# Performance work log

Hardware: AMD Instinct MI355X
Metric: run time of the kernel (lower is better)

Reference implementation:

```python
import jax, jax.numpy as jnp
import numpy as np

N_NODES = 50000
N_EDGES = 800000
IN_CH, HID_CH, OUT_CH = 128, 128, 64


def _gcn_conv(x, W, b, src, dst, n):
    """PyG GCNConv: self-loops + symmetric norm + linear + scatter-add + bias."""
    loop = jnp.arange(n, dtype=src.dtype)
    src_sl = jnp.concatenate([src, loop])  # [E+N]
    dst_sl = jnp.concatenate([dst, loop])
    # degree computed on edges incl. self-loops (edge weight 1)
    deg = jax.ops.segment_sum(jnp.ones_like(dst_sl, dtype=x.dtype), dst_sl,
                              num_segments=n)
    dinv = jnp.where(deg > 0, jax.lax.rsqrt(deg), 0.0)
    norm = dinv[src_sl] * dinv[dst_sl]  # [E+N]
    xw = x @ W  # [N, F_out]
    msg = xw[src_sl] * norm[:, None]  # gather + scale, [E+N, F_out]
    out = jax.ops.segment_sum(msg, dst_sl, num_segments=n)
    return out + b


def setup_inputs() -> dict:
    key = jax.random.key(0)
    ks = jax.random.split(key, 5)
    x = jax.random.normal(ks[0], (N_NODES, IN_CH), dtype=jnp.float32)
    edge_index = jax.random.randint(ks[1], (2, N_EDGES), 0, N_NODES, dtype=jnp.int64)
    s1 = 1.0 / np.sqrt(IN_CH)
    s2 = 1.0 / np.sqrt(HID_CH)
    W1 = jax.random.normal(ks[2], (IN_CH, HID_CH), dtype=jnp.float32) * s1
    W2 = jax.random.normal(ks[3], (HID_CH, HID_CH), dtype=jnp.float32) * s2
    W3 = jax.random.normal(ks[4], (HID_CH, OUT_CH), dtype=jnp.float32) * s2
    return {
        "x": x, "edge_index": edge_index,
        "W1": W1, "b1": jnp.zeros((HID_CH,), jnp.float32),
        "W2": W2, "b2": jnp.zeros((HID_CH,), jnp.float32),
        "W3": W3, "b3": jnp.zeros((OUT_CH,), jnp.float32),
    }


def reference(x, edge_index, W1, b1, W2, b2, W3, b3):
    n = x.shape[0]
    src, dst = edge_index[0], edge_index[1]
    # dropout(p=0.6) is identity in eval mode
    h = jax.nn.relu(_gcn_conv(x, W1, b1, src, dst, n))
    h = jax.nn.relu(_gcn_conv(h, W2, b2, src, dst, n))
    out = _gcn_conv(h, W3, b3, src, dst, n)
    return out
```

## Files before the change

### kernel.cpp

```cpp
#include <hip/hip_runtime.h>
#include <cstdint>

#define CAP 32768
#define CHUNK 2048

typedef __attribute__((ext_vector_type(8))) short bf8_t;
typedef __attribute__((ext_vector_type(4))) float f4_t;

__device__ __forceinline__ uint32_t f_to_bf(float f) {
    union { float f; uint32_t u; } v; v.f = f;
    uint32_t u = v.u;
    return (u + 0x7fffu + ((u >> 16) & 1u)) >> 16;
}
__device__ __forceinline__ float bf_to_f(uint32_t h) {
    union { uint32_t u; float f; } v; v.u = h << 16; return v.f;
}
__device__ __forceinline__ float2 bf2_to_f2(uint32_t u) {
    union { uint32_t u; float f; } a, b;
    a.u = u << 16; b.u = u & 0xffff0000u;
    float2 r; r.x = a.f; r.y = b.f; return r;
}
__device__ __forceinline__ void fma8(float* acc, uint4 u, float d) {
    float2 p0 = bf2_to_f2(u.x), p1 = bf2_to_f2(u.y);
    float2 p2 = bf2_to_f2(u.z), p3 = bf2_to_f2(u.w);
    acc[0] += p0.x * d; acc[1] += p0.y * d;
    acc[2] += p1.x * d; acc[3] += p1.y * d;
    acc[4] += p2.x * d; acc[5] += p2.y * d;
    acc[6] += p3.x * d; acc[7] += p3.y * d;
}

__device__ __forceinline__ int detect64(const int* __restrict__ e32) {
    return (e32[1] | e32[3] | e32[5] | e32[7]) == 0;
}
__device__ __forceinline__ int edge_at(const void* edges, int is64, int idx) {
    if (is64) return (int)((const long long*)edges)[idx];
    return ((const int*)edges)[idx];
}

__device__ __forceinline__ void wsplit_body(
    int idx, const float* __restrict__ W1, const float* __restrict__ W2,
    const float* __restrict__ W3,
    uint16_t* w1h, uint16_t* w1l, uint16_t* w2h, uint16_t* w2l,
    uint16_t* w3h, uint16_t* w3l) {
    const float* W; uint16_t* oh; uint16_t* ol; int FOUT; int e;
    if (idx < 16384)      { W = W1; oh = w1h; ol = w1l; FOUT = 128; e = idx; }
    else if (idx < 32768) { W = W2; oh = w2h; ol = w2l; FOUT = 128; e = idx - 16384; }
    else                  { W = W3; oh = w3h; ol = w3l; FOUT = 64;  e = idx - 32768; }
    int j = e & 7;
    int lane = (e >> 3) & 63;
    int rem = e >> 9;
    int NT = FOUT >> 4;
    int nt = rem % NT, kc = rem / NT;
    int k = kc * 32 + ((lane >> 4) << 3) + j;
    int c = nt * 16 + (lane & 15);
    float v = W[(size_t)k * FOUT + c];
    uint32_t h = f_to_bf(v);
    uint32_t l = f_to_bf(v - bf_to_f(h));
    oh[e] = (uint16_t)h;
    ol[e] = (uint16_t)l;
}

__global__ __launch_bounds__(256) void scatter_wprep_kernel(
    const void* __restrict__ ei, int* __restrict__ bucket_cur,
    int2* __restrict__ buckets, int E, int sbcnt,
    const float* __restrict__ W1, const float* __restrict__ W2,
    const float* __restrict__ W3,
    uint16_t* w1h, uint16_t* w1l, uint16_t* w2h, uint16_t* w2l,
    uint16_t* w3h, uint16_t* w3l) {
    int tid = threadIdx.x;
    if ((int)blockIdx.x >= sbcnt) {
        int idx = (blockIdx.x - sbcnt) * 256 + tid;
        wsplit_body(idx, W1, W2, W3, w1h, w1l, w2h, w2l, w3h, w3l);
        return;
    }
    __shared__ int cnt[64];
    int base = blockIdx.x * CHUNK;
    int is64 = detect64((const int*)ei);
    if (tid < 64) cnt[tid] = 0;
    __syncthreads();
    int dloc[8], sloc[8];
#pragma unroll
    for (int it = 0; it < 8; it++) {
        int i = base + it * 256 + tid;
        int d = (i < E) ? edge_at(ei, is64, E + i) : -1;
        int s = (i < E) ? edge_at(ei, is64, i) : 0;
        dloc[it] = d;
        sloc[it] = s;
        if (d >= 0) atomicAdd(&cnt[d >> 10], 1);
    }
    __syncthreads();
    if (tid < 64) {
        int v = cnt[tid];
        cnt[tid] = atomicAdd(&bucket_cur[tid], v);
    }
    __syncthreads();
#pragma unroll
    for (int it = 0; it < 8; it++) {
        if (dloc[it] >= 0) {
            int b = dloc[it] >> 10;
            int p = atomicAdd(&cnt[b], 1);
            buckets[(size_t)b * CAP + p] = make_int2(sloc[it], dloc[it]);
        }
    }
}

__device__ __forceinline__ void gemm1_body(
    const float* __restrict__ A, const uint16_t* __restrict__ Wfhi,
    const uint16_t* __restrict__ Wflo, uint16_t* __restrict__ Yout,
    int n, int wid, int tile0, int tstride, int lane,
    uint16_t* __restrict__ hs, uint16_t* __restrict__ ls) {
    constexpr int NT = 8, NTW = 2, LDW = 136;
    int ntiles = (n + 15) >> 4;
    bf8_t wh[NTW][4], wl[NTW][4];
#pragma unroll
    for (int t = 0; t < NTW; t++) {
        int nt = wid * NTW + t;
#pragma unroll
        for (int kc = 0; kc < 4; kc++) {
            size_t b = ((size_t)(kc * NT + nt) * 64 + lane) * 8;
            wh[t][kc] = *(const bf8_t*)&Wfhi[b];
            wl[t][kc] = *(const bf8_t*)&Wflo[b];
        }
    }
    int row_in = lane & 15;
    int koff = (lane >> 4) << 3;
    int colb = lane & 15;
    int rq = (lane >> 4) << 2;
    int kcw = wid;
    float4 pv = {0, 0, 0, 0}, qv = {0, 0, 0, 0};
    if (tile0 < ntiles) {
        int arow = (tile0 << 4) + row_in; if (arow >= n) arow = n - 1;
        const float* ap = A + (size_t)arow * 128 + kcw * 32 + koff;
        pv = *(const float4*)ap;
        qv = *(const float4*)(ap + 4);
    }
    for (int tile = tile0; tile < ntiles; tile += tstride) {
        int R = tile << 4;
        {
            float vv[8] = {pv.x, pv.y, pv.z, pv.w, qv.x, qv.y, qv.z, qv.w};
            bf8_t H, L;
#pragma unroll
            for (int j = 0; j < 8; j++) {
                uint32_t h = f_to_bf(vv[j]);
                H[j] = (short)h;
                L[j] = (short)f_to_bf(vv[j] - bf_to_f(h));
            }
            *(bf8_t*)&hs[row_in * LDW + kcw * 32 + koff] = H;
            *(bf8_t*)&ls[row_in * LDW + kcw * 32 + koff] = L;
        }
        __syncthreads();
        int tnext = tile + tstride;
        if (tnext < ntiles) {
            int arow2 = (tnext << 4) + row_in; if (arow2 >= n) arow2 = n - 1;
            const float* ap2 = A + (size_t)arow2 * 128 + kcw * 32 + koff;
            pv = *(const float4*)ap2;
            qv = *(const float4*)(ap2 + 4);
        }
        bf8_t ah[4], al[4];
#pragma unroll
        for (int kc = 0; kc < 4; kc++) {
            ah[kc] = *(const bf8_t*)&hs[(lane & 15) * LDW + koff + kc * 32];
            al[kc] = *(const bf8_t*)&ls[(lane & 15) * LDW + koff + kc * 32];
        }
        f4_t acc[NTW];
#pragma unroll
        for (int t = 0; t < NTW; t++) acc[t] = (f4_t){0.f, 0.f, 0.f, 0.f};
#pragma unroll
        for (int kc = 0; kc < 4; kc++) {
#pragma unroll
            for (int t = 0; t < NTW; t++) {
                acc[t] = __builtin_amdgcn_mfma_f32_16x16x32_bf16(ah[kc], wh[t][kc], acc[t], 0, 0, 0);
                acc[t] = __builtin_amdgcn_mfma_f32_16x16x32_bf16(ah[kc], wl[t][kc], acc[t], 0, 0, 0);
                acc[t] = __builtin_amdgcn_mfma_f32_16x16x32_bf16(al[kc], wh[t][kc], acc[t], 0, 0, 0);
            }
        }
#pragma unroll
        for (int t = 0; t < NTW; t++) {
            int c = (wid * NTW + t) * 16 + colb;
#pragma unroll
            for (int r = 0; r < 4; r++) {
                int row = R + rq + r;
                if (row < n)
                    Yout[(size_t)row * 128 + c] = (uint16_t)f_to_bf(acc[t][r]);
            }
        }
        __syncthreads();
    }
}

__global__ __launch_bounds__(256) void csrfill_gemm1_kernel(
    const int2* __restrict__ buckets, const int* __restrict__ bucket_cur,
    int* __restrict__ row_ptr, int* __restrict__ col,
    float* __restrict__ dinv, int nbuck,
    const float* __restrict__ x, const uint16_t* __restrict__ w1h,
    const uint16_t* __restrict__ w1l, uint16_t* __restrict__ y1, int n) {
    __shared__ __align__(16) char smem[12288];
    __shared__ int s_bo;
    int tid = threadIdx.x;
    if ((int)blockIdx.x >= nbuck) {
        uint16_t* hs = (uint16_t*)smem;
        uint16_t* ls = (uint16_t*)(smem + 4352);
        int lane = tid & 63, wid = tid >> 6;
        gemm1_body(x, w1h, w1l, y1, n, wid, blockIdx.x - nbuck,
                   gridDim.x - nbuck, lane, hs, ls);
        return;
    }
    int* cnt = (int*)smem;
    int* sb  = (int*)(smem + 4096);
    int* cur = (int*)(smem + 8192);
    int b = blockIdx.x;
    int base = b << 10;
    int lim = min(1024, n - base);
    if (tid < 64) {
        int v = (tid < nbuck) ? bucket_cur[tid] : 0;
        int incl = v;
#pragma unroll
        for (int off = 1; off < 64; off <<= 1) {
            int t = __shfl_up(incl, off);
            if (tid >= off) incl += t;
        }
        int tot = __shfl(incl, nbuck - 1);
        int bo = (b > 0) ? __shfl(incl, b - 1) : 0;
        if (tid == 0) {
            s_bo = bo;
            if (b == nbuck - 1) row_ptr[n] = tot;
        }
    }
    int ecnt = bucket_cur[b];
    const int2* ebase = buckets + (size_t)b * CAP;
    for (int i = tid; i < 1024; i += 256) cnt[i] = 0;
    __syncthreads();
    {
        int i = tid;
        for (; i + 768 < ecnt; i += 1024) {
            int y0 = ebase[i].y;
            int y1_ = ebase[i + 256].y;
            int y2_ = ebase[i + 512].y;
            int y3_ = ebase[i + 768].y;
            atomicAdd(&cnt[y0 - base], 1);
            atomicAdd(&cnt[y1_ - base], 1);
            atomicAdd(&cnt[y2_ - base], 1);
            atomicAdd(&cnt[y3_ - base], 1);
        }
        for (; i < ecnt; i += 256)
            atomicAdd(&cnt[ebase[i].y - base], 1);
    }
    __syncthreads();
    for (int i = tid; i < lim; i += 256)
        dinv[base + i] = rsqrtf((float)(cnt[i] + 1));
    __syncthreads();
    int* a = cnt; int* s = sb;
    for (int st = 1; st < 1024; st <<= 1) {
        for (int i = tid; i < 1024; i += 256)
            s[i] = a[i] + ((i >= st) ? a[i - st] : 0);
        __syncthreads();
        int* t = a; a = s; s = t;
    }
    int bo = s_bo;
    for (int i = tid; i < lim; i += 256) {
        int v = ((i > 0) ? a[i - 1] : 0) + bo;
        row_ptr[base + i] = v;
        cur[i] = v;
    }
    __syncthreads();
    {
        int i = tid;
        for (; i + 768 < ecnt; i += 1024) {
            int2 e0 = ebase[i];
            int2 e1 = ebase[i + 256];
            int2 e2 = ebase[i + 512];
            int2 e3 = ebase[i + 768];
            int p0 = atomicAdd(&cur[e0.y - base], 1); col[p0] = e0.x;
            int p1 = atomicAdd(&cur[e1.y - base], 1); col[p1] = e1.x;
            int p2 = atomicAdd(&cur[e2.y - base], 1); col[p2] = e2.x;
            int p3 = atomicAdd(&cur[e3.y - base], 1); col[p3] = e3.x;
        }
        for (; i < ecnt; i += 256) {
            int2 e = ebase[i];
            int p = atomicAdd(&cur[e.y - base], 1);
            col[p] = e.x;
        }
    }
}

template <int FOUT, bool SRC_SCALE>
__global__ __launch_bounds__(256) void agg_gemm_kernel(
    const uint16_t* __restrict__ Yin, const int* __restrict__ row_ptr,
    const int* __restrict__ col, const float* __restrict__ dinv,
    const float* __restrict__ bias,
    const uint16_t* __restrict__ Wfhi, const uint16_t* __restrict__ Wflo,
    uint16_t* __restrict__ Yout, int n) {
    __shared__ uint4 hs4[16 * 17];
    __shared__ uint4 ls4[16 * 17];
    int tid = threadIdx.x, wid = tid >> 6, lane = tid & 63;
    int base = blockIdx.x * 16;
    int g = lane & 15, j = lane >> 4;
    const uint4* Y4 = (const uint4*)Yin;

    float4 bb0 = *(const float4*)&bias[g * 8];
    float4 bb1 = *(const float4*)&bias[g * 8 + 4];
    float bb[8] = {bb0.x, bb0.y, bb0.z, bb0.w, bb1.x, bb1.y, bb1.z, bb1.w};

    for (int q = 0; q < 4; q++) {
        int r = wid * 4 + q, node = base + r;
        uint4 ph = (uint4){0, 0, 0, 0}, pl = (uint4){0, 0, 0, 0};
        if (node < n) {
            float di = dinv[node];
            float aA[8] = {}, aB[8] = {};
            {
                float sd = (j == 0) ? (SRC_SCALE ? di : 1.f) : 0.f;
                uint4 su = Y4[(size_t)node * 16 + g];
                fma8(aA, su, sd);
            }
            int start = row_ptr[node], end = row_ptr[node + 1];
            for (int b = start; b < end; b += 64) {
                int cnt = min(64, end - b);
                int sv = (b + lane < end) ? col[b + lane] : 0;
                for (int k = 0; k < cnt; k += 8) {
                    int iA = k + j, iB = k + 4 + j;
                    int sA = __shfl(sv, iA & 63);
                    int sB = __shfl(sv, iB & 63);
                    float dA = (iA < cnt) ? (SRC_SCALE ? dinv[sA] : 1.f) : 0.f;
                    float dB = (iB < cnt) ? (SRC_SCALE ? dinv[sB] : 1.f) : 0.f;
                    uint4 uA = Y4[(size_t)sA * 16 + g];
                    uint4 uB = Y4[(size_t)sB * 16 + g];
                    fma8(aA, uA, dA);
                    fma8(aB, uB, dB);
                }
            }
            float o[8];
#pragma unroll
            for (int t = 0; t < 8; t++) o[t] = aA[t] + aB[t];
#pragma unroll
            for (int t = 0; t < 8; t++) o[t] += __shfl_xor(o[t], 16);
#pragma unroll
            for (int t = 0; t < 8; t++) o[t] += __shfl_xor(o[t], 32);
            uint32_t hh[8];
#pragma unroll
            for (int t = 0; t < 8; t++) {
                o[t] = fmaxf(o[t] * di + bb[t], 0.f);
                hh[t] = f_to_bf(o[t]);
            }
            ph = (uint4){hh[0] | (hh[1] << 16), hh[2] | (hh[3] << 16),
                         hh[4] | (hh[5] << 16), hh[6] | (hh[7] << 16)};
            uint32_t ll[8];
#pragma unroll
            for (int t = 0; t < 8; t++) ll[t] = f_to_bf(o[t] - bf_to_f(hh[t]));
            pl = (uint4){ll[0] | (ll[1] << 16), ll[2] | (ll[3] << 16),
                         ll[4] | (ll[5] << 16), ll[6] | (ll[7] << 16)};
        }
        if (j == 0) {
            hs4[r * 17 + g] = ph;
            ls4[r * 17 + g] = pl;
        }
    }
    __syncthreads();

    const uint16_t* hs = (const uint16_t*)hs4;
    const uint16_t* ls = (const uint16_t*)ls4;
    constexpr int NT = FOUT / 16;
    constexpr int NTW = NT / 4;
    constexpr int LDW = 136;
    int cp = wid;
    bf8_t wh[NTW][4], wl[NTW][4];
#pragma unroll
    for (int t = 0; t < NTW; t++) {
        int nt = cp * NTW + t;
#pragma unroll
        for (int kc = 0; kc < 4; kc++) {
            size_t b = ((size_t)(kc * NT + nt) * 64 + lane) * 8;
            wh[t][kc] = *(const bf8_t*)&Wfhi[b];
            wl[t][kc] = *(const bf8_t*)&Wflo[b];
        }
    }
    int koff = (lane >> 4) << 3;
    int colb = lane & 15;
    int rq = (lane >> 4) << 2;
    bf8_t ah[4], al[4];
#pragma unroll
    for (int kc = 0; kc < 4; kc++) {
        ah[kc] = *(const bf8_t*)(hs + (lane & 15) * LDW + koff + kc * 32);
        al[kc] = *(const bf8_t*)(ls + (lane & 15) * LDW + koff + kc * 32);
    }
    f4_t acc[NTW];
#pragma unroll
    for (int t = 0; t < NTW; t++) acc[t] = (f4_t){0.f, 0.f, 0.f, 0.f};
#pragma unroll
    for (int kc = 0; kc < 4; kc++) {
#pragma unroll
        for (int t = 0; t < NTW; t++) {
            acc[t] = __builtin_amdgcn_mfma_f32_16x16x32_bf16(ah[kc], wh[t][kc], acc[t], 0, 0, 0);
            acc[t] = __builtin_amdgcn_mfma_f32_16x16x32_bf16(ah[kc], wl[t][kc], acc[t], 0, 0, 0);
            acc[t] = __builtin_amdgcn_mfma_f32_16x16x32_bf16(al[kc], wh[t][kc], acc[t], 0, 0, 0);
        }
    }
#pragma unroll
    for (int t = 0; t < NTW; t++) {
        int c = (cp * NTW + t) * 16 + colb;
#pragma unroll
        for (int r = 0; r < 4; r++) {
            int row = base + rq + r;
            if (row < n) {
                float v = acc[t][r] * dinv[row];
                Yout[(size_t)row * FOUT + c] = (uint16_t)f_to_bf(v);
            }
        }
    }
}

__global__ __launch_bounds__(256) void agg_final_kernel(
    const uint16_t* __restrict__ Y, const int* __restrict__ row_ptr,
    const int* __restrict__ col, const float* __restrict__ dinv,
    const float* __restrict__ bias, float* __restrict__ out, int n) {
    int w = blockIdx.x * 4 + (threadIdx.x >> 6);
    int lane = threadIdx.x & 63;
    if (w >= n) return;
    int g = lane & 7, j = lane >> 3;
    const uint4* Y4 = (const uint4*)Y;
    float4 bb0 = *(const float4*)&bias[g * 8];
    float4 bb1 = *(const float4*)&bias[g * 8 + 4];
    float bb[8] = {bb0.x, bb0.y, bb0.z, bb0.w, bb1.x, bb1.y, bb1.z, bb1.w};

    float aA[8] = {}, aB[8] = {};
    {
        uint4 su = Y4[(size_t)w * 8 + g];
        fma8(aA, su, (j == 0) ? 1.f : 0.f);
    }
    int start = row_ptr[w], end = row_ptr[w + 1];
    for (int b = start; b < end; b += 64) {
        int cnt = min(64, end - b);
        int sv = (b + lane < end) ? col[b + lane] : 0;
        for (int k = 0; k < cnt; k += 16) {
            int iA = k + j, iB = k + 8 + j;
            int sA = __shfl(sv, iA & 63);
            int sB = __shfl(sv, iB & 63);
            float dA = (iA < cnt) ? 1.f : 0.f;
            float dB = (iB < cnt) ? 1.f : 0.f;
            uint4 uA = Y4[(size_t)sA * 8 + g];
            uint4 uB = Y4[(size_t)sB * 8 + g];
            fma8(aA, uA, dA);
            fma8(aB, uB, dB);
        }
    }
    float o[8];
#pragma unroll
    for (int t = 0; t < 8; t++) o[t] = aA[t] + aB[t];
#pragma unroll
    for (int t = 0; t < 8; t++) o[t] += __shfl_xor(o[t], 8);
#pragma unroll
    for (int t = 0; t < 8; t++) o[t] += __shfl_xor(o[t], 16);
#pragma unroll
    for (int t = 0; t < 8; t++) o[t] += __shfl_xor(o[t], 32);
    float di = dinv[w];
#pragma unroll
    for (int t = 0; t < 8; t++) o[t] = o[t] * di + bb[t];
    if (j == 0) {
        float4 o0 = {o[0], o[1], o[2], o[3]};
        float4 o1 = {o[4], o[5], o[6], o[7]};
        *(float4*)&out[(size_t)w * 64 + g * 8] = o0;
        *(float4*)&out[(size_t)w * 64 + g * 8 + 4] = o1;
    }
}

extern "C" void kernel_launch(void* const* d_in, const int* in_sizes, int n_in,
                              void* d_out, int out_size, void* d_ws, size_t ws_size,
                              hipStream_t stream) {
    const float* x  = (const float*)d_in[0];
    const void*  ei = d_in[1];
    const float* W1 = (const float*)d_in[2];
    const float* b1 = (const float*)d_in[3];
    const float* W2 = (const float*)d_in[4];
    const float* b2 = (const float*)d_in[5];
    const float* W3 = (const float*)d_in[6];
    const float* b3 = (const float*)d_in[7];
    int n = in_sizes[0] / 128;
    int E = in_sizes[1] / 2;
    int nbuck = (n + 1023) >> 10;

    char* p = (char*)d_ws;
    auto carve = [&](size_t bytes) {
        char* r = p;
        p += (bytes + 255) & ~(size_t)255;
        return r;
    };
    float*    dinv       = (float*)carve((size_t)n * 4);
    int*      row_ptr    = (int*)carve((size_t)(n + 1) * 4);
    int*      bucket_cur = (int*)carve(64 * 4);
    int*      col        = (int*)carve((size_t)E * 4);
    int2*     buckets    = (int2*)carve((size_t)64 * CAP * 8);
    uint16_t* y1         = (uint16_t*)carve((size_t)n * 128 * 2);
    uint16_t* y2         = (uint16_t*)carve((size_t)n * 128 * 2);
    uint16_t* y3         = (uint16_t*)carve((size_t)n * 64 * 2);
    uint16_t* w1h        = (uint16_t*)carve(128 * 128 * 2);
    uint16_t* w1l        = (uint16_t*)carve(128 * 128 * 2);
    uint16_t* w2h        = (uint16_t*)carve(128 * 128 * 2);
    uint16_t* w2l        = (uint16_t*)carve(128 * 128 * 2);
    uint16_t* w3h        = (uint16_t*)carve(128 * 64 * 2);
    uint16_t* w3l        = (uint16_t*)carve(128 * 64 * 2);

    int sbcnt = (E + CHUNK - 1) / CHUNK;
    int fb = (n + 15) / 16;

    hipMemsetAsync(bucket_cur, 0, 64 * 4, stream);
    scatter_wprep_kernel<<<sbcnt + 160, 256, 0, stream>>>(
        ei, bucket_cur, buckets, E, sbcnt,
        W1, W2, W3, w1h, w1l, w2h, w2l, w3h, w3l);
    csrfill_gemm1_kernel<<<nbuck + 782, 256, 0, stream>>>(
        buckets, bucket_cur, row_ptr, col, dinv, nbuck,
        x, w1h, w1l, y1, n);
    agg_gemm_kernel<128, true><<<fb, 256, 0, stream>>>(
        y1, row_ptr, col, dinv, b1, w2h, w2l, y2, n);
    agg_gemm_kernel<64, false><<<fb, 256, 0, stream>>>(
        y2, row_ptr, col, dinv, b2, w3h, w3l, y3, n);
    agg_final_kernel<<<(n + 3) / 4, 256, 0, stream>>>(
        y3, row_ptr, col, dinv, b3, (float*)d_out, n);
}
```

Measured before the change: 230.4 us.

## Reformulate neighbor aggregation as sparse-weight MFMA over staged edge rows

The per-node gather-and-FMA aggregation is replaced by a block-wide scheme. Chunks of 64 CSR edges for the block's 16 nodes are staged into shared memory, a 16x64 selection matrix of bf16 hi/lo edge weights is built, and the aggregation runs as MFMA products, with self-loops handled as a diagonal pass. This aims to move the aggregation onto matrix cores and improve gather coalescing. In exchange it adds several __syncthreads per chunk, shared-memory zeroing, a binary search per edge, and strided transposed LDS reads for the B fragments.

```diff
diff --git a/kernel.cpp b/kernel.cpp
--- a/kernel.cpp
+++ b/kernel.cpp
@@ -290,118 +290,195 @@
     const float* __restrict__ bias,
     const uint16_t* __restrict__ Wfhi, const uint16_t* __restrict__ Wflo,
     uint16_t* __restrict__ Yout, int n) {
-    __shared__ uint4 hs4[16 * 17];
-    __shared__ uint4 ls4[16 * 17];
+    constexpr int RLD = 136;
+    constexpr int SLD = 72;
+    __shared__ uint16_t rows[64 * RLD];
+    __shared__ uint16_t Shi[16 * SLD];
+    __shared__ uint16_t Slo[16 * SLD];
+    __shared__ uint16_t hs[16 * 136];
+    __shared__ uint16_t ls[16 * 136];
+    __shared__ int   s_rp[17];
+    __shared__ float s_di[16];
+    __shared__ float s_bias[128];
+
     int tid = threadIdx.x, wid = tid >> 6, lane = tid & 63;
     int base = blockIdx.x * 16;
-    int g = lane & 15, j = lane >> 4;
+    int grp = lane & 15;
     const uint4* Y4 = (const uint4*)Yin;
 
-    float4 bb0 = *(const float4*)&bias[g * 8];
-    float4 bb1 = *(const float4*)&bias[g * 8 + 4];
-    float bb[8] = {bb0.x, bb0.y, bb0.z, bb0.w, bb1.x, bb1.y, bb1.z, bb1.w};
-
-    for (int q = 0; q < 4; q++) {
-        int r = wid * 4 + q, node = base + r;
-        uint4 ph = (uint4){0, 0, 0, 0}, pl = (uint4){0, 0, 0, 0};
-        if (node < n) {
-            float di = dinv[node];
-            float aA[8] = {}, aB[8] = {};
-            {
-                float sd = (j == 0) ? (SRC_SCALE ? di : 1.f) : 0.f;
-                uint4 su = Y4[(size_t)node * 16 + g];
-                fma8(aA, su, sd);
-            }
-            int start = row_ptr[node], end = row_ptr[node + 1];
-            for (int b = start; b < end; b += 64) {
-                int cnt = min(64, end - b);
-                int sv = (b + lane < end) ? col[b + lane] : 0;
-                for (int k = 0; k < cnt; k += 8) {
-                    int iA = k + j, iB = k + 4 + j;
-                    int sA = __shfl(sv, iA & 63);
-                    int sB = __shfl(sv, iB & 63);
-                    float dA = (iA < cnt) ? (SRC_SCALE ? dinv[sA] : 1.f) : 0.f;
-                    float dB = (iB < cnt) ? (SRC_SCALE ? dinv[sB] : 1.f) : 0.f;
-                    uint4 uA = Y4[(size_t)sA * 16 + g];
-                    uint4 uB = Y4[(size_t)sB * 16 + g];
-                    fma8(aA, uA, dA);
-                    fma8(aB, uB, dB);
+    if (tid < 17) {
+        int idx = base + tid; if (idx > n) idx = n;
+        s_rp[tid] = row_ptr[idx];
+    }
+    if (tid >= 32 && tid < 48) {
+        int m = tid - 32;
+        s_di[m] = (base + m < n) ? dinv[base + m] : 0.f;
+    }
+    if (tid >= 64 && tid < 192) s_bias[tid - 64] = bias[tid - 64];
+    {
+        uint4* r4 = (uint4*)rows;
+        for (int i = tid; i < 64 * RLD / 8; i += 256) r4[i] = (uint4){0, 0, 0, 0};
+    }
+    __syncthreads();
+
+    int e0 = s_rp[0], e1 = s_rp[16];
+    f4_t acc[2] = {(f4_t){0.f, 0.f, 0.f, 0.f}, (f4_t){0.f, 0.f, 0.f, 0.f}};
+
+    for (int cb = e0; cb < e1; cb += 64) {
+        int cnt = min(64, e1 - cb);
+        int sv = (cb + lane < e1) ? col[cb + lane] : 0;
+        for (int i = tid; i < (16 * SLD) / 8; i += 256) {
+            ((uint4*)Shi)[i] = (uint4){0, 0, 0, 0};
+            ((uint4*)Slo)[i] = (uint4){0, 0, 0, 0};
+        }
+        __syncthreads();
+        if (wid == 0 && lane < cnt) {
+            int e = cb + lane;
+            int lo = 0, hi = 16;
+            while (hi - lo > 1) {
+                int mid = (lo + hi) >> 1;
+                if (s_rp[mid] <= e) lo = mid; else hi = mid;
+            }
+            float w = SRC_SCALE ? dinv[sv] : 1.f;
+            uint32_t h = f_to_bf(w);
+            Shi[lo * SLD + lane] = (uint16_t)h;
+            if (SRC_SCALE)
+                Slo[lo * SLD + lane] = (uint16_t)f_to_bf(w - bf_to_f(h));
+        }
+#pragma unroll
+        for (int i = 0; i < 4; i++) {
+            int slot = wid * 16 + i * 4 + (lane >> 4);
+            int src = __shfl(sv, slot);
+            if (slot < cnt) {
+                uint4 u = Y4[(size_t)src * 16 + grp];
+                *(uint4*)&rows[slot * RLD + grp * 8] = u;
+            }
+        }
+        __syncthreads();
+#pragma unroll
+        for (int t = 0; t < 2; t++) {
+            int nt = wid * 2 + t;
+#pragma unroll
+            for (int kc = 0; kc < 2; kc++) {
+                int kb = kc * 32 + ((lane >> 4) << 3);
+                bf8_t bfrag;
+#pragma unroll
+                for (int j = 0; j < 8; j++)
+                    bfrag[j] = (short)rows[(kb + j) * RLD + nt * 16 + grp];
+                bf8_t ah = *(const bf8_t*)&Shi[grp * SLD + kb];
+                acc[t] = __builtin_amdgcn_mfma_f32_16x16x32_bf16(ah, bfrag, acc[t], 0, 0, 0);
+                if (SRC_SCALE) {
+                    bf8_t al = *(const bf8_t*)&Slo[grp * SLD + kb];
+                    acc[t] = __builtin_amdgcn_mfma_f32_16x16x32_bf16(al, bfrag, acc[t], 0, 0, 0);
                 }
             }
-            float o[8];
-#pragma unroll
-            for (int t = 0; t < 8; t++) o[t] = aA[t] + aB[t];
-#pragma unroll
-            for (int t = 0; t < 8; t++) o[t] += __shfl_xor(o[t], 16);
-#pragma unroll
-            for (int t = 0; t < 8; t++) o[t] += __shfl_xor(o[t], 32);
-            uint32_t hh[8];
-#pragma unroll
-            for (int t = 0; t < 8; t++) {
-                o[t] = fmaxf(o[t] * di + bb[t], 0.f);
-                hh[t] = f_to_bf(o[t]);
-            }
-            ph = (uint4){hh[0] | (hh[1] << 16), hh[2] | (hh[3] << 16),
-                         hh[4] | (hh[5] << 16), hh[6] | (hh[7] << 16)};
-            uint32_t ll[8];
-#pragma unroll
-            for (int t = 0; t < 8; t++) ll[t] = f_to_bf(o[t] - bf_to_f(hh[t]));
-            pl = (uint4){ll[0] | (ll[1] << 16), ll[2] | (ll[3] << 16),
-                         ll[4] | (ll[5] << 16), ll[6] | (ll[7] << 16)};
-        }
-        if (j == 0) {
-            hs4[r * 17 + g] = ph;
-            ls4[r * 17 + g] = pl;
-        }
-    }
-    __syncthreads();
-
-    const uint16_t* hs = (const uint16_t*)hs4;
-    const uint16_t* ls = (const uint16_t*)ls4;
+        }
+        __syncthreads();
+    }
+
+    {
+        for (int i = tid; i < (16 * SLD) / 8; i += 256) {
+            ((uint4*)Shi)[i] = (uint4){0, 0, 0, 0};
+            ((uint4*)Slo)[i] = (uint4){0, 0, 0, 0};
+        }
+        __syncthreads();
+        if (wid == 0 && lane < 16) {
+            float w = SRC_SCALE ? s_di[lane] : 1.f;
+            uint32_t h = f_to_bf(w);
+            Shi[lane * SLD + lane] = (uint16_t)h;
+            if (SRC_SCALE)
+                Slo[lane * SLD + lane] = (uint16_t)f_to_bf(w - bf_to_f(h));
+        }
+        {
+            int slot = wid * 4 + (lane >> 4);
+            int node = base + slot;
+            if (node < n) {
+                uint4 u = Y4[(size_t)node * 16 + grp];
+                *(uint4*)&rows[slot * RLD + grp * 8] = u;
+            } else {
+                *(uint4*)&rows[slot * RLD + grp * 8] = (uint4){0, 0, 0, 0};
+            }
+        }
+        __syncthreads();
+#pragma unroll
+        for (int t = 0; t < 2; t++) {
+            int nt = wid * 2 + t;
+            int kb = (lane >> 4) << 3;
+            bf8_t bfrag;
+#pragma unroll
+            for (int j = 0; j < 8; j++)
+                bfrag[j] = (short)rows[(kb + j) * RLD + nt * 16 + grp];
+            bf8_t ah = *(const bf8_t*)&Shi[grp * SLD + kb];
+            acc[t] = __builtin_amdgcn_mfma_f32_16x16x32_bf16(ah, bfrag, acc[t], 0, 0, 0);
+            if (SRC_SCALE) {
+                bf8_t al = *(const bf8_t*)&Slo[grp * SLD + kb];
+                acc[t] = __builtin_amdgcn_mfma_f32_16x16x32_bf16(al, bfrag, acc[t], 0, 0, 0);
+            }
+        }
+    }
+
+    {
+        int rq = (lane >> 4) << 2;
+#pragma unroll
+        for (int t = 0; t < 2; t++) {
+            int nt = wid * 2 + t;
+            int ch = nt * 16 + grp;
+            float bb = s_bias[ch];
+#pragma unroll
+            for (int r = 0; r < 4; r++) {
+                int m = rq + r;
+                float v = fmaxf(acc[t][r] * s_di[m] + bb, 0.f);
+                uint32_t h = f_to_bf(v);
+                hs[m * 136 + ch] = (uint16_t)h;
+                ls[m * 136 + ch] = (uint16_t)f_to_bf(v - bf_to_f(h));
+            }
+        }
+    }
+    __syncthreads();
+
     constexpr int NT = FOUT / 16;
     constexpr int NTW = NT / 4;
     constexpr int LDW = 136;
     int cp = wid;
-    bf8_t wh[NTW][4], wl[NTW][4];
+    bf8_t wwh[NTW][4], wwl[NTW][4];
 #pragma unroll
     for (int t = 0; t < NTW; t++) {
         int nt = cp * NTW + t;
 #pragma unroll
         for (int kc = 0; kc < 4; kc++) {
             size_t b = ((size_t)(kc * NT + nt) * 64 + lane) * 8;
-            wh[t][kc] = *(const bf8_t*)&Wfhi[b];
-            wl[t][kc] = *(const bf8_t*)&Wflo[b];
+            wwh[t][kc] = *(const bf8_t*)&Wfhi[b];
+            wwl[t][kc] = *(const bf8_t*)&Wflo[b];
         }
     }
     int koff = (lane >> 4) << 3;
-    int colb = lane & 15;
     int rq = (lane >> 4) << 2;
-    bf8_t ah[4], al[4];
+    bf8_t gah[4], gal[4];
 #pragma unroll
     for (int kc = 0; kc < 4; kc++) {
-        ah[kc] = *(const bf8_t*)(hs + (lane & 15) * LDW + koff + kc * 32);
-        al[kc] = *(const bf8_t*)(ls + (lane & 15) * LDW + koff + kc * 32);
-    }
-    f4_t acc[NTW];
-#pragma unroll
-    for (int t = 0; t < NTW; t++) acc[t] = (f4_t){0.f, 0.f, 0.f, 0.f};
+        gah[kc] = *(const bf8_t*)&hs[grp * LDW + koff + kc * 32];
+        gal[kc] = *(const bf8_t*)&ls[grp * LDW + koff + kc * 32];
+    }
+    f4_t gacc[NTW];
+#pragma unroll
+    for (int t = 0; t < NTW; t++) gacc[t] = (f4_t){0.f, 0.f, 0.f, 0.f};
 #pragma unroll
     for (int kc = 0; kc < 4; kc++) {
 #pragma unroll
         for (int t = 0; t < NTW; t++) {
-            acc[t] = __builtin_amdgcn_mfma_f32_16x16x32_bf16(ah[kc], wh[t][kc], acc[t], 0, 0, 0);
-            acc[t] = __builtin_amdgcn_mfma_f32_16x16x32_bf16(ah[kc], wl[t][kc], acc[t], 0, 0, 0);
-            acc[t] = __builtin_amdgcn_mfma_f32_16x16x32_bf16(al[kc], wh[t][kc], acc[t], 0, 0, 0);
+            gacc[t] = __builtin_amdgcn_mfma_f32_16x16x32_bf16(gah[kc], wwh[t][kc], gacc[t], 0, 0, 0);
+            gacc[t] = __builtin_amdgcn_mfma_f32_16x16x32_bf16(gah[kc], wwl[t][kc], gacc[t], 0, 0, 0);
+            gacc[t] = __builtin_amdgcn_mfma_f32_16x16x32_bf16(gal[kc], wwh[t][kc], gacc[t], 0, 0, 0);
         }
     }
 #pragma unroll
     for (int t = 0; t < NTW; t++) {
-        int c = (cp * NTW + t) * 16 + colb;
+        int c = (cp * NTW + t) * 16 + grp;
 #pragma unroll
         for (int r = 0; r < 4; r++) {
             int row = base + rq + r;
             if (row < n) {
-                float v = acc[t][r] * dinv[row];
+                float v = gacc[t][r] * s_di[rq + r];
                 Yout[(size_t)row * FOUT + c] = (uint16_t)f_to_bf(v);
             }
         }
```

Result: slower. 249.6 us (+8.3%).
